# Performance work log

Hardware: AMD Instinct MI355X
Metric: run time of the kernel (lower is better)

Reference implementation:

```python
import jax, jax.numpy as jnp
import numpy as np

GROUP = 128  # per-group quantization along the input dimension


def _quantize_int4(w):
    """Asymmetric INT4 per-group quantization. w: [out, in] -> (q, scale, zero).
    q: int32 in [0,15], shape [out, in//GROUP, GROUP]; scale/zero: [out, in//GROUP]."""
    o, i = w.shape
    wg = w.reshape(o, i // GROUP, GROUP)
    mn = wg.min(axis=-1)
    mx = wg.max(axis=-1)
    scale = (mx - mn) / 15.0
    scale = jnp.where(scale == 0, jnp.float32(1.0), scale)
    zero = jnp.clip(jnp.round(-mn / scale), 0.0, 15.0)
    q = jnp.clip(jnp.round(wg / scale[..., None]) + zero[..., None], 0.0, 15.0).astype(jnp.int32)
    return q, scale.astype(jnp.float32), zero.astype(jnp.float32)


def _dequant(q, s, z):
    """(q - zero) * scale, regrouped back to [out, in]."""
    w = (q.astype(jnp.float32) - z[..., None]) * s[..., None]
    return w.reshape(q.shape[0], -1)


def setup_inputs() -> dict:
    key = jax.random.key(0)
    ks = jax.random.split(key, 5)
    B, D_IN, D_H, D_OUT = 512, 2048, 8192, 2048
    x = jax.random.normal(ks[0], (B, D_IN), dtype=jnp.float32)
    w1 = jax.random.normal(ks[1], (D_H, D_IN), dtype=jnp.float32) * 0.02
    b1 = jax.random.normal(ks[2], (D_H,), dtype=jnp.float32) * 0.01
    w2 = jax.random.normal(ks[3], (D_OUT, D_H), dtype=jnp.float32) * 0.02
    b2 = jax.random.normal(ks[4], (D_OUT,), dtype=jnp.float32) * 0.01
    q1, s1, z1 = _quantize_int4(w1)
    q2, s2, z2 = _quantize_int4(w2)
    return {"x": x, "q1": q1, "s1": s1, "z1": z1, "b1": b1,
            "q2": q2, "s2": s2, "z2": z2, "b2": b2}


def reference(x, q1, s1, z1, b1, q2, s2, z2, b2):
    # Layer 1: INT4 dequant + Linear + ReLU (fused in the native kernel)
    w1 = _dequant(q1, s1, z1)              # [D_H, D_IN]
    h = jax.nn.relu(x @ w1.T + b1)         # [B, D_H]
    # Layer 2: INT4 dequant + Linear (no activation)
    w2 = _dequant(q2, s2, z2)              # [D_OUT, D_H]
    return h @ w2.T + b2                   # [B, D_OUT]
```

## Files before the change

kernel.cpp:

```cpp
#include <hip/hip_runtime.h>
#include <stdint.h>

typedef unsigned short u16;
typedef __attribute__((ext_vector_type(8))) short bf16x8;
typedef __attribute__((ext_vector_type(8))) unsigned short u16x8;
typedef __attribute__((ext_vector_type(4))) float f32x4;
typedef __attribute__((ext_vector_type(4))) int i32x4;

__device__ __forceinline__ u16 f2bf(float f) {
  uint32_t u = __builtin_bit_cast(uint32_t, f);
  u += 0x7fffu + ((u >> 16) & 1u);
  return (u16)(u >> 16);
}

#define GLD16(g, l)                                                         \
  __builtin_amdgcn_global_load_lds(                                         \
      (const __attribute__((address_space(1))) void*)(g),                   \
      (__attribute__((address_space(3))) void*)(l), 16, 0, 0)


__global__ __launch_bounds__(256) void cvt_f32_bf16(const float* __restrict__ src,
                                                    u16* __restrict__ dst, int n8) {
  int t = blockIdx.x * 256 + threadIdx.x;
  if (t >= n8) return;
  f32x4 a = ((const f32x4*)src)[2 * t];
  f32x4 b = ((const f32x4*)src)[2 * t + 1];
  u16x8 o;
  o[0] = f2bf(a[0]); o[1] = f2bf(a[1]); o[2] = f2bf(a[2]); o[3] = f2bf(a[3]);
  o[4] = f2bf(b[0]); o[5] = f2bf(b[1]); o[6] = f2bf(b[2]); o[7] = f2bf(b[3]);
  ((u16x8*)dst)[t] = o;
}

__global__ __launch_bounds__(256) void dequant_w(const int* __restrict__ q,
                                                 const float* __restrict__ s,
                                                 const float* __restrict__ z,
                                                 u16* __restrict__ w, int n8) {
  int t = blockIdx.x * 256 + threadIdx.x;
  if (t >= n8) return;
  int g = t >> 4;
  float sc = s[g];
  float zp = z[g];
  i32x4 a = ((const i32x4*)q)[2 * t];
  i32x4 b = ((const i32x4*)q)[2 * t + 1];
  u16x8 o;
  o[0] = f2bf(((float)a[0] - zp) * sc);
  o[1] = f2bf(((float)a[1] - zp) * sc);
  o[2] = f2bf(((float)a[2] - zp) * sc);
  o[3] = f2bf(((float)a[3] - zp) * sc);
  o[4] = f2bf(((float)b[0] - zp) * sc);
  o[5] = f2bf(((float)b[1] - zp) * sc);
  o[6] = f2bf(((float)b[2] - zp) * sc);
  o[7] = f2bf(((float)b[3] - zp) * sc);
  ((u16x8*)w)[t] = o;
}

__global__ __launch_bounds__(256) void bias_init(float* __restrict__ out,
                                                 const float* __restrict__ b,
                                                 int N, int n4) {
  int t = blockIdx.x * 256 + threadIdx.x;
  if (t >= n4) return;
  int idx = t * 4;
  int n = idx & (N - 1);
  *(f32x4*)(out + idx) = *(const f32x4*)(b + n);
}

template <bool RELU, bool OUT_BF16, bool ATOMIC>
__global__ __launch_bounds__(256) void gemm_bt(const u16* __restrict__ A,
                                               const u16* __restrict__ Bm,
                                               const float* __restrict__ bias,
                                               void* __restrict__ Cout,
                                               int M, int N, int K, int kChunk) {
  __shared__ u16 As[128 * 32];
  __shared__ u16 Bs[128 * 32];
  const int tid = threadIdx.x;
  const int wave = tid >> 6;
  const int lane = tid & 63;
  const int m0 = blockIdx.y << 7;
  const int n0 = blockIdx.x << 7;
  const int kStart = blockIdx.z * kChunk;
  const int srow = lane >> 2;
  const int scol = (lane & 3) << 3;
  const int wm = (wave >> 1) << 6;
  const int wn = (wave & 1) << 6;
  const int quad = lane >> 4;
  const int l15 = lane & 15;

  const u16* Ab = A + (size_t)(m0 + 32 * wave + srow) * K + kStart + scol;
  const u16* Bb = Bm + (size_t)(n0 + 32 * wave + srow) * K + kStart + scol;
  u16* AsD0 = &As[(32 * wave + 0) * 32];
  u16* AsD1 = &As[(32 * wave + 16) * 32];
  u16* BsD0 = &Bs[(32 * wave + 0) * 32];
  u16* BsD1 = &Bs[(32 * wave + 16) * 32];
  const size_t rowskip = (size_t)16 * K;

  f32x4 acc[4][4];
#pragma unroll
  for (int i = 0; i < 4; i++)
#pragma unroll
    for (int j = 0; j < 4; j++) acc[i][j] = (f32x4){0.f, 0.f, 0.f, 0.f};

  for (int k = 0; k < kChunk; k += 32) {
    GLD16(Ab + k, AsD0);
    GLD16(Ab + k + rowskip, AsD1);
    GLD16(Bb + k, BsD0);
    GLD16(Bb + k + rowskip, BsD1);
    __syncthreads();
    bf16x8 af[4], bf[4];
#pragma unroll
    for (int i = 0; i < 4; i++)
      af[i] = *(const bf16x8*)&As[(wm + i * 16 + l15) * 32 + quad * 8];
#pragma unroll
    for (int j = 0; j < 4; j++)
      bf[j] = *(const bf16x8*)&Bs[(wn + j * 16 + l15) * 32 + quad * 8];
#pragma unroll
    for (int i = 0; i < 4; i++)
#pragma unroll
      for (int j = 0; j < 4; j++)
        acc[i][j] = __builtin_amdgcn_mfma_f32_16x16x32_bf16(af[i], bf[j], acc[i][j], 0, 0, 0);
    __syncthreads();
  }

#pragma unroll
  for (int i = 0; i < 4; i++) {
#pragma unroll
    for (int j = 0; j < 4; j++) {
      const int col = n0 + wn + j * 16 + l15;
      float bv = 0.f;
      if (!ATOMIC) bv = bias[col];
#pragma unroll
      for (int r = 0; r < 4; r++) {
        const int row = m0 + wm + i * 16 + quad * 4 + r;
        float v = acc[i][j][r];
        if (ATOMIC) {
          atomicAdd((float*)Cout + (size_t)row * N + col, v);
        } else {
          v += bv;
          if (RELU) v = v > 0.f ? v : 0.f;
          if (OUT_BF16)
            ((u16*)Cout)[(size_t)row * N + col] = f2bf(v);
          else
            ((float*)Cout)[(size_t)row * N + col] = v;
        }
      }
    }
  }
}


extern "C" void kernel_launch(void* const* d_in, const int* in_sizes, int n_in,
                              void* d_out, int out_size, void* d_ws, size_t ws_size,
                              hipStream_t stream) {
  const float* x  = (const float*)d_in[0];
  const int*   q1 = (const int*)d_in[1];
  const float* s1 = (const float*)d_in[2];
  const float* z1 = (const float*)d_in[3];
  const float* b1 = (const float*)d_in[4];
  const int*   q2 = (const int*)d_in[5];
  const float* s2 = (const float*)d_in[6];
  const float* z2 = (const float*)d_in[7];
  const float* b2 = (const float*)d_in[8];
  float* out = (float*)d_out;

  const int B = 512, D_IN = 2048, D_H = 8192, D_OUT = 2048;

  char* ws = (char*)d_ws;
  u16* xb  = (u16*)(ws);
  u16* w1b = (u16*)(ws + (size_t)2 * 1024 * 1024);
  u16* hb  = (u16*)(ws + (size_t)34 * 1024 * 1024);
  u16* w2b = (u16*)(ws + (size_t)42 * 1024 * 1024);

  cvt_f32_bf16<<<(B * D_IN / 8 + 255) / 256, 256, 0, stream>>>(x, xb, B * D_IN / 8);
  dequant_w<<<(D_H * D_IN / 8 + 255) / 256, 256, 0, stream>>>(q1, s1, z1, w1b, D_H * D_IN / 8);
  dequant_w<<<(D_OUT * D_H / 8 + 255) / 256, 256, 0, stream>>>(q2, s2, z2, w2b, D_OUT * D_H / 8);
  dim3 g1(D_H / 128, B / 128, 1);
  gemm_bt<true, true, false><<<g1, 256, 0, stream>>>(xb, w1b, b1, hb, B, D_H, D_IN, D_IN);
  bias_init<<<(B * D_OUT / 4 + 255) / 256, 256, 0, stream>>>(out, b2, D_OUT, B * D_OUT / 4);
  dim3 g2(D_OUT / 128, B / 128, 4);
  gemm_bt<false, false, true><<<g2, 256, 0, stream>>>(hb, w2b, nullptr, out, B, D_OUT, D_H, D_H / 4);
}
```

Measured before the change: 276.1 us.

## Fuse INT4 dequantization into both GEMMs with fp16 MFMA and double-buffered LDS

```diff
diff --git a/kernel.cpp b/kernel.cpp
--- a/kernel.cpp
+++ b/kernel.cpp
@@ -2,160 +2,236 @@
 #include <stdint.h>
 
 typedef unsigned short u16;
-typedef __attribute__((ext_vector_type(8))) short bf16x8;
-typedef __attribute__((ext_vector_type(8))) unsigned short u16x8;
+typedef _Float16 f16;
+typedef __attribute__((ext_vector_type(8))) _Float16 f16x8;
 typedef __attribute__((ext_vector_type(4))) float f32x4;
 typedef __attribute__((ext_vector_type(4))) int i32x4;
 
-__device__ __forceinline__ u16 f2bf(float f) {
-  uint32_t u = __builtin_bit_cast(uint32_t, f);
-  u += 0x7fffu + ((u >> 16) & 1u);
-  return (u16)(u >> 16);
-}
-
-#define GLD16(g, l)                                                         \
-  __builtin_amdgcn_global_load_lds(                                         \
-      (const __attribute__((address_space(1))) void*)(g),                   \
-      (__attribute__((address_space(3))) void*)(l), 16, 0, 0)
-
-
-__global__ __launch_bounds__(256) void cvt_f32_bf16(const float* __restrict__ src,
-                                                    u16* __restrict__ dst, int n8) {
+#define LW 56
+#define LWI 28
+
+#define BARRIER() asm volatile("s_waitcnt lgkmcnt(0)\n\ts_barrier" ::: "memory")
+
+__device__ __forceinline__ int pk2(float a, float b) {
+  return __builtin_bit_cast(int, __builtin_amdgcn_cvt_pkrtz(a, b));
+}
+
+
+__global__ __launch_bounds__(256) void cvt_x(const float* __restrict__ src,
+                                             i32x4* __restrict__ dst, int n8) {
   int t = blockIdx.x * 256 + threadIdx.x;
   if (t >= n8) return;
   f32x4 a = ((const f32x4*)src)[2 * t];
   f32x4 b = ((const f32x4*)src)[2 * t + 1];
-  u16x8 o;
-  o[0] = f2bf(a[0]); o[1] = f2bf(a[1]); o[2] = f2bf(a[2]); o[3] = f2bf(a[3]);
-  o[4] = f2bf(b[0]); o[5] = f2bf(b[1]); o[6] = f2bf(b[2]); o[7] = f2bf(b[3]);
-  ((u16x8*)dst)[t] = o;
-}
-
-__global__ __launch_bounds__(256) void dequant_w(const int* __restrict__ q,
-                                                 const float* __restrict__ s,
-                                                 const float* __restrict__ z,
-                                                 u16* __restrict__ w, int n8) {
-  int t = blockIdx.x * 256 + threadIdx.x;
-  if (t >= n8) return;
-  int g = t >> 4;
-  float sc = s[g];
-  float zp = z[g];
-  i32x4 a = ((const i32x4*)q)[2 * t];
-  i32x4 b = ((const i32x4*)q)[2 * t + 1];
-  u16x8 o;
-  o[0] = f2bf(((float)a[0] - zp) * sc);
-  o[1] = f2bf(((float)a[1] - zp) * sc);
-  o[2] = f2bf(((float)a[2] - zp) * sc);
-  o[3] = f2bf(((float)a[3] - zp) * sc);
-  o[4] = f2bf(((float)b[0] - zp) * sc);
-  o[5] = f2bf(((float)b[1] - zp) * sc);
-  o[6] = f2bf(((float)b[2] - zp) * sc);
-  o[7] = f2bf(((float)b[3] - zp) * sc);
-  ((u16x8*)w)[t] = o;
+  i32x4 o = {pk2(a[0], a[1]), pk2(a[2], a[3]), pk2(b[0], b[1]), pk2(b[2], b[3])};
+  dst[t] = o;
 }
 
 __global__ __launch_bounds__(256) void bias_init(float* __restrict__ out,
-                                                 const float* __restrict__ b,
-                                                 int N, int n4) {
+                                                 const float* __restrict__ b, int n4) {
   int t = blockIdx.x * 256 + threadIdx.x;
   if (t >= n4) return;
   int idx = t * 4;
-  int n = idx & (N - 1);
-  *(f32x4*)(out + idx) = *(const f32x4*)(b + n);
-}
-
-template <bool RELU, bool OUT_BF16, bool ATOMIC>
-__global__ __launch_bounds__(256) void gemm_bt(const u16* __restrict__ A,
-                                               const u16* __restrict__ Bm,
-                                               const float* __restrict__ bias,
-                                               void* __restrict__ Cout,
-                                               int M, int N, int K, int kChunk) {
-  __shared__ u16 As[128 * 32];
-  __shared__ u16 Bs[128 * 32];
+  *(f32x4*)(out + idx) = *(const f32x4*)(b + (idx & 2047));
+}
+
+__global__ __launch_bounds__(256, 2) void gemm1(const u16* __restrict__ X,
+                                                const int* __restrict__ Q,
+                                                const float* __restrict__ S,
+                                                const float* __restrict__ Z,
+                                                const float* __restrict__ bias,
+                                                f16* __restrict__ H) {
+  const int K = 2048, N = 8192, G = 16;
+  __shared__ int As[2][64 * LWI];
+  __shared__ int Bs[2][128 * LWI];
   const int tid = threadIdx.x;
-  const int wave = tid >> 6;
-  const int lane = tid & 63;
-  const int m0 = blockIdx.y << 7;
-  const int n0 = blockIdx.x << 7;
-  const int kStart = blockIdx.z * kChunk;
-  const int srow = lane >> 2;
-  const int scol = (lane & 3) << 3;
-  const int wm = (wave >> 1) << 6;
-  const int wn = (wave & 1) << 6;
-  const int quad = lane >> 4;
-  const int l15 = lane & 15;
-
-  const u16* Ab = A + (size_t)(m0 + 32 * wave + srow) * K + kStart + scol;
-  const u16* Bb = Bm + (size_t)(n0 + 32 * wave + srow) * K + kStart + scol;
-  u16* AsD0 = &As[(32 * wave + 0) * 32];
-  u16* AsD1 = &As[(32 * wave + 16) * 32];
-  u16* BsD0 = &Bs[(32 * wave + 0) * 32];
-  u16* BsD1 = &Bs[(32 * wave + 16) * 32];
-  const size_t rowskip = (size_t)16 * K;
-
-  f32x4 acc[4][4];
-#pragma unroll
-  for (int i = 0; i < 4; i++)
+  const int wave = tid >> 6, lane = tid & 63, quad = lane >> 4, l15 = lane & 15;
+  const int m0 = blockIdx.y << 6, n0 = blockIdx.x << 7;
+  const int wm = (wave >> 1) << 5, wn = (wave & 1) << 6;
+  const int arow = tid >> 2, ak = (tid & 3) << 3;
+  const int brow = tid >> 1, bk = (tid & 1) << 4;
+
+  const u16* ap = X + (size_t)(m0 + arow) * K + ak;
+  const int* qp = Q + (size_t)(n0 + brow) * K + bk;
+  const float* sp = S + (n0 + brow) * G;
+  const float* zp = Z + (n0 + brow) * G;
+
+  i32x4 nq0 = *(const i32x4*)(qp);
+  i32x4 nq1 = *(const i32x4*)(qp + 4);
+  i32x4 nq2 = *(const i32x4*)(qp + 8);
+  i32x4 nq3 = *(const i32x4*)(qp + 12);
+  i32x4 na = *(const i32x4*)(ap);
+  float ns = sp[0], nz = zp[0];
+
+  f32x4 acc[2][4];
+#pragma unroll
+  for (int i = 0; i < 2; i++)
 #pragma unroll
     for (int j = 0; j < 4; j++) acc[i][j] = (f32x4){0.f, 0.f, 0.f, 0.f};
 
-  for (int k = 0; k < kChunk; k += 32) {
-    GLD16(Ab + k, AsD0);
-    GLD16(Ab + k + rowskip, AsD1);
-    GLD16(Bb + k, BsD0);
-    GLD16(Bb + k + rowskip, BsD1);
-    __syncthreads();
-    bf16x8 af[4], bf[4];
-#pragma unroll
-    for (int i = 0; i < 4; i++)
-      af[i] = *(const bf16x8*)&As[(wm + i * 16 + l15) * 32 + quad * 8];
+#pragma unroll 2
+  for (int k = 0; k < K; k += 32) {
+    const int buf = (k >> 5) & 1;
+    i32x4 q0 = nq0, q1 = nq1, q2 = nq2, q3 = nq3, av = na;
+    const float f = ns, o = -nz * ns;
+    if (k + 32 < K) {
+      nq0 = *(const i32x4*)(qp + k + 32);
+      nq1 = *(const i32x4*)(qp + k + 36);
+      nq2 = *(const i32x4*)(qp + k + 40);
+      nq3 = *(const i32x4*)(qp + k + 44);
+      na = *(const i32x4*)(ap + k + 32);
+      const int g = (k + 32) >> 7;
+      ns = sp[g];
+      nz = zp[g];
+    }
+    i32x4 lo = {pk2(fmaf((float)q0[0], f, o), fmaf((float)q0[1], f, o)),
+                pk2(fmaf((float)q0[2], f, o), fmaf((float)q0[3], f, o)),
+                pk2(fmaf((float)q1[0], f, o), fmaf((float)q1[1], f, o)),
+                pk2(fmaf((float)q1[2], f, o), fmaf((float)q1[3], f, o))};
+    i32x4 hi = {pk2(fmaf((float)q2[0], f, o), fmaf((float)q2[1], f, o)),
+                pk2(fmaf((float)q2[2], f, o), fmaf((float)q2[3], f, o)),
+                pk2(fmaf((float)q3[0], f, o), fmaf((float)q3[1], f, o)),
+                pk2(fmaf((float)q3[2], f, o), fmaf((float)q3[3], f, o))};
+    *(i32x4*)&Bs[buf][brow * LWI + (bk >> 1)] = lo;
+    *(i32x4*)&Bs[buf][brow * LWI + (bk >> 1) + 4] = hi;
+    *(i32x4*)&As[buf][arow * LWI + (ak >> 1)] = av;
+    BARRIER();
+    const f16* AsH = (const f16*)As[buf];
+    const f16* BsH = (const f16*)Bs[buf];
+    f16x8 af[2], bf[4];
+#pragma unroll
+    for (int i = 0; i < 2; i++)
+      af[i] = *(const f16x8*)&AsH[(wm + i * 16 + l15) * LW + quad * 8];
 #pragma unroll
     for (int j = 0; j < 4; j++)
-      bf[j] = *(const bf16x8*)&Bs[(wn + j * 16 + l15) * 32 + quad * 8];
-#pragma unroll
-    for (int i = 0; i < 4; i++)
+      bf[j] = *(const f16x8*)&BsH[(wn + j * 16 + l15) * LW + quad * 8];
+#pragma unroll
+    for (int i = 0; i < 2; i++)
 #pragma unroll
       for (int j = 0; j < 4; j++)
-        acc[i][j] = __builtin_amdgcn_mfma_f32_16x16x32_bf16(af[i], bf[j], acc[i][j], 0, 0, 0);
-    __syncthreads();
+        acc[i][j] = __builtin_amdgcn_mfma_f32_16x16x32_f16(af[i], bf[j], acc[i][j], 0, 0, 0);
   }
 
 #pragma unroll
-  for (int i = 0; i < 4; i++) {
+  for (int i = 0; i < 2; i++)
 #pragma unroll
     for (int j = 0; j < 4; j++) {
       const int col = n0 + wn + j * 16 + l15;
-      float bv = 0.f;
-      if (!ATOMIC) bv = bias[col];
+      const float bv = bias[col];
 #pragma unroll
       for (int r = 0; r < 4; r++) {
         const int row = m0 + wm + i * 16 + quad * 4 + r;
-        float v = acc[i][j][r];
-        if (ATOMIC) {
-          atomicAdd((float*)Cout + (size_t)row * N + col, v);
-        } else {
-          v += bv;
-          if (RELU) v = v > 0.f ? v : 0.f;
-          if (OUT_BF16)
-            ((u16*)Cout)[(size_t)row * N + col] = f2bf(v);
-          else
-            ((float*)Cout)[(size_t)row * N + col] = v;
-        }
+        float v = acc[i][j][r] + bv;
+        v = v > 0.f ? v : 0.f;
+        H[(size_t)row * N + col] = (f16)v;
       }
     }
+}
+
+__global__ __launch_bounds__(256, 2) void gemm2(const u16* __restrict__ Hm,
+                                                const int* __restrict__ Q,
+                                                const float* __restrict__ S,
+                                                const float* __restrict__ Z,
+                                                float* __restrict__ out) {
+  const int K = 8192, N = 2048, G = 64, KCH = 1024;
+  __shared__ int As[2][128 * LWI];
+  __shared__ int Bs[2][128 * LWI];
+  const int tid = threadIdx.x;
+  const int wave = tid >> 6, lane = tid & 63, quad = lane >> 4, l15 = lane & 15;
+  const int m0 = blockIdx.y << 7, n0 = blockIdx.x << 7;
+  const int kStart = blockIdx.z << 10;
+  const int wm = (wave >> 1) << 6, wn = (wave & 1) << 6;
+  const int arow = tid >> 1, ak = (tid & 1) << 4;
+  const int brow = tid >> 1, bk = (tid & 1) << 4;
+
+  const u16* ap = Hm + (size_t)(m0 + arow) * K + kStart + ak;
+  const int* qp = Q + (size_t)(n0 + brow) * K + kStart + bk;
+  const float* sp = S + (n0 + brow) * G;
+  const float* zp = Z + (n0 + brow) * G;
+  const int g0 = kStart >> 7;
+
+  i32x4 nq0 = *(const i32x4*)(qp);
+  i32x4 nq1 = *(const i32x4*)(qp + 4);
+  i32x4 nq2 = *(const i32x4*)(qp + 8);
+  i32x4 nq3 = *(const i32x4*)(qp + 12);
+  i32x4 na0 = *(const i32x4*)(ap);
+  i32x4 na1 = *(const i32x4*)(ap + 8);
+  float ns = sp[g0], nz = zp[g0];
+
+  f32x4 acc[4][4];
+#pragma unroll
+  for (int i = 0; i < 4; i++)
+#pragma unroll
+    for (int j = 0; j < 4; j++) acc[i][j] = (f32x4){0.f, 0.f, 0.f, 0.f};
+
+#pragma unroll 2
+  for (int k = 0; k < KCH; k += 32) {
+    const int buf = (k >> 5) & 1;
+    i32x4 q0 = nq0, q1 = nq1, q2 = nq2, q3 = nq3, a0 = na0, a1 = na1;
+    const float f = ns, o = -nz * ns;
+    if (k + 32 < KCH) {
+      nq0 = *(const i32x4*)(qp + k + 32);
+      nq1 = *(const i32x4*)(qp + k + 36);
+      nq2 = *(const i32x4*)(qp + k + 40);
+      nq3 = *(const i32x4*)(qp + k + 44);
+      na0 = *(const i32x4*)(ap + k + 32);
+      na1 = *(const i32x4*)(ap + k + 40);
+      const int g = (kStart + k + 32) >> 7;
+      ns = sp[g];
+      nz = zp[g];
+    }
+    i32x4 lo = {pk2(fmaf((float)q0[0], f, o), fmaf((float)q0[1], f, o)),
+                pk2(fmaf((float)q0[2], f, o), fmaf((float)q0[3], f, o)),
+                pk2(fmaf((float)q1[0], f, o), fmaf((float)q1[1], f, o)),
+                pk2(fmaf((float)q1[2], f, o), fmaf((float)q1[3], f, o))};
+    i32x4 hi = {pk2(fmaf((float)q2[0], f, o), fmaf((float)q2[1], f, o)),
+                pk2(fmaf((float)q2[2], f, o), fmaf((float)q2[3], f, o)),
+                pk2(fmaf((float)q3[0], f, o), fmaf((float)q3[1], f, o)),
+                pk2(fmaf((float)q3[2], f, o), fmaf((float)q3[3], f, o))};
+    *(i32x4*)&Bs[buf][brow * LWI + (bk >> 1)] = lo;
+    *(i32x4*)&Bs[buf][brow * LWI + (bk >> 1) + 4] = hi;
+    *(i32x4*)&As[buf][arow * LWI + (ak >> 1)] = a0;
+    *(i32x4*)&As[buf][arow * LWI + (ak >> 1) + 4] = a1;
+    BARRIER();
+    const f16* AsH = (const f16*)As[buf];
+    const f16* BsH = (const f16*)Bs[buf];
+    f16x8 af[4], bf[4];
+#pragma unroll
+    for (int i = 0; i < 4; i++)
+      af[i] = *(const f16x8*)&AsH[(wm + i * 16 + l15) * LW + quad * 8];
+#pragma unroll
+    for (int j = 0; j < 4; j++)
+      bf[j] = *(const f16x8*)&BsH[(wn + j * 16 + l15) * LW + quad * 8];
+#pragma unroll
+    for (int i = 0; i < 4; i++)
+#pragma unroll
+      for (int j = 0; j < 4; j++)
+        acc[i][j] = __builtin_amdgcn_mfma_f32_16x16x32_f16(af[i], bf[j], acc[i][j], 0, 0, 0);
   }
+
+#pragma unroll
+  for (int i = 0; i < 4; i++)
+#pragma unroll
+    for (int j = 0; j < 4; j++) {
+      const int col = n0 + wn + j * 16 + l15;
+#pragma unroll
+      for (int r = 0; r < 4; r++) {
+        const int row = m0 + wm + i * 16 + quad * 4 + r;
+        atomicAdd(out + (size_t)row * N + col, acc[i][j][r]);
+      }
+    }
 }
 
 
 extern "C" void kernel_launch(void* const* d_in, const int* in_sizes, int n_in,
                               void* d_out, int out_size, void* d_ws, size_t ws_size,
                               hipStream_t stream) {
-  const float* x  = (const float*)d_in[0];
-  const int*   q1 = (const int*)d_in[1];
+  const float* x = (const float*)d_in[0];
+  const int* q1 = (const int*)d_in[1];
   const float* s1 = (const float*)d_in[2];
   const float* z1 = (const float*)d_in[3];
   const float* b1 = (const float*)d_in[4];
-  const int*   q2 = (const int*)d_in[5];
+  const int* q2 = (const int*)d_in[5];
   const float* s2 = (const float*)d_in[6];
   const float* z2 = (const float*)d_in[7];
   const float* b2 = (const float*)d_in[8];
@@ -164,17 +240,15 @@
   const int B = 512, D_IN = 2048, D_H = 8192, D_OUT = 2048;
 
   char* ws = (char*)d_ws;
-  u16* xb  = (u16*)(ws);
-  u16* w1b = (u16*)(ws + (size_t)2 * 1024 * 1024);
-  u16* hb  = (u16*)(ws + (size_t)34 * 1024 * 1024);
-  u16* w2b = (u16*)(ws + (size_t)42 * 1024 * 1024);
-
-  cvt_f32_bf16<<<(B * D_IN / 8 + 255) / 256, 256, 0, stream>>>(x, xb, B * D_IN / 8);
-  dequant_w<<<(D_H * D_IN / 8 + 255) / 256, 256, 0, stream>>>(q1, s1, z1, w1b, D_H * D_IN / 8);
-  dequant_w<<<(D_OUT * D_H / 8 + 255) / 256, 256, 0, stream>>>(q2, s2, z2, w2b, D_OUT * D_H / 8);
-  dim3 g1(D_H / 128, B / 128, 1);
-  gemm_bt<true, true, false><<<g1, 256, 0, stream>>>(xb, w1b, b1, hb, B, D_H, D_IN, D_IN);
-  bias_init<<<(B * D_OUT / 4 + 255) / 256, 256, 0, stream>>>(out, b2, D_OUT, B * D_OUT / 4);
-  dim3 g2(D_OUT / 128, B / 128, 4);
-  gemm_bt<false, false, true><<<g2, 256, 0, stream>>>(hb, w2b, nullptr, out, B, D_OUT, D_H, D_H / 4);
-}
+  u16* xh = (u16*)ws;
+  u16* h = (u16*)(ws + (size_t)2 * 1024 * 1024);
+
+  cvt_x<<<(B * D_IN / 8 + 255) / 256, 256, 0, stream>>>(x, (i32x4*)xh, B * D_IN / 8);
+  bias_init<<<(B * D_OUT / 4 + 255) / 256, 256, 0, stream>>>(out, b2, B * D_OUT / 4);
+
+  dim3 g1(D_H / 128, B / 64, 1);
+  gemm1<<<g1, 256, 0, stream>>>(xh, q1, s1, z1, b1, (f16*)h);
+
+  dim3 g2(D_OUT / 128, B / 128, 8);
+  gemm2<<<g2, 256, 0, stream>>>(h, q2, s2, z2, out);
+}
```

Result: slower. 291.1 us (+5.4%).
